# Optimization experiments

Hardware: AMD Instinct MI355X
Metric: run time of the kernel (lower is better)

## Reference

```python
import jax, jax.numpy as jnp
import numpy as np

EEG_CH = 64      # eeg_channel_new
WIN = 128        # window_length
KEN = 10         # cnn_ken_num
CONV_H = 64      # cnn_conv_hight (stride/kernel height)


def setup_inputs() -> dict:
    key = jax.random.key(0)
    ks = jax.random.split(key, 11)
    n = jax.random.normal
    return {
        "x": n(ks[0], (1, 1, 66, 128), dtype=jnp.float32),
        # SE fcn: Linear(64,64) -> Tanh -> Linear(64,64) -> Sigmoid -> Softmax
        "se_w1": n(ks[1], (64, 64), dtype=jnp.float32) * 0.1,
        "se_b1": n(ks[2], (64,), dtype=jnp.float32) * 0.1,
        "se_w2": n(ks[3], (64, 64), dtype=jnp.float32) * 0.1,
        "se_b2": n(ks[4], (64,), dtype=jnp.float32) * 0.1,
        # Conv2d(1, 10, (64, 9), stride=(64, 1))
        "conv_w": n(ks[5], (10, 1, 64, 9), dtype=jnp.float32) * 0.05,
        "conv_b": n(ks[6], (10,), dtype=jnp.float32) * 0.05,
        # fcn: Linear(20,10) -> Sigmoid -> Linear(10,2) -> Softmax
        "fcn_w1": n(ks[7], (10, 20), dtype=jnp.float32) * 0.1,
        "fcn_b1": n(ks[8], (10,), dtype=jnp.float32) * 0.1,
        "fcn_w2": n(ks[9], (2, 10), dtype=jnp.float32) * 0.1,
        "fcn_b2": n(ks[10], (2,), dtype=jnp.float32) * 0.1,
    }


def _dot(a, b):
    # Faithful to torch: tensordot over dim 0 -> [64,1]; diag of non-square -> [1];
    # then broadcast-divide by per-column norms -> [64].
    temp = jnp.diagonal(jnp.tensordot(a, b, axes=[[0], [0]]))  # [1]
    norm_a = jnp.linalg.norm(a, axis=0)                        # [64]
    norm_b = jnp.linalg.norm(b, axis=0)                        # [1]
    return temp / (norm_a * norm_b)                            # [64]


def reference(x, se_w1, se_b1, se_w2, se_b2, conv_w, conv_b,
              fcn_w1, fcn_b1, fcn_w2, fcn_b2):
    eeg = x[:, :, 1:1 + EEG_CH, :]      # [1,1,64,128]
    wav_a = x[:, :, 0:1, :]             # [1,1,1,128]
    wav_b = x[:, :, -1:, :]             # [1,1,1,128]

    e2 = eeg.reshape(EEG_CH, WIN)       # [64,128]
    r_a = _dot(e2.T, wav_a.reshape(1, WIN).T)   # [64]
    r_b = _dot(e2.T, wav_b.reshape(1, WIN).T)   # [64]
    eeg_r = jnp.concatenate([r_a, r_b]).reshape(2, -1)  # [2,64]

    # SE channel attention
    h = jnp.tanh(eeg_r @ se_w1.T + se_b1)
    se_w = jax.nn.softmax(jax.nn.sigmoid(h @ se_w2.T + se_b2), axis=1)  # [2,64]
    sd = eeg.reshape(1, EEG_CH, WIN).transpose(1, 0, 2)  # [64,1,128]
    sd = jnp.concatenate([sd, sd], axis=0)               # [128,1,128]
    # (transpose(0,2) * w.view(1,-1)).transpose(0,2) == scale along doubled-channel dim
    eeg_se = (sd * se_w.reshape(-1)[:, None, None]).transpose(1, 0, 2)  # [1,128,128]

    y = eeg_se.reshape(1, 1, 2 * EEG_CH, WIN)            # [1,1,128,128]
    y = jax.lax.conv_general_dilated(
        y, conv_w, window_strides=(CONV_H, 1), padding='VALID',
        dimension_numbers=('NCHW', 'OIHW', 'NCHW'))       # [1,10,2,120]
    y = jax.nn.relu(y + conv_b[None, :, None, None])
    # AdaptiveAvgPool2d((2,1)): H already 2, mean over W
    y = jnp.mean(y, axis=3, keepdims=True)                # [1,10,2,1]
    y = y.reshape(1, -1)                                  # [1,20]

    h2 = jax.nn.sigmoid(y @ fcn_w1.T + fcn_b1)
    return jax.nn.softmax(h2 @ fcn_w2.T + fcn_b2, axis=1)  # [1,2]
```

## Files before the change

kernel.cpp:

```cpp
#include <hip/hip_runtime.h>
#include <math.h>

#define EEG_CH 64
#define WIN    128
#define KW     9
#define OUTW   120
#define NOUT   10
#define ROWP   132
#define CWP    12

__device__ float        g_msum[2 * NOUT];
__device__ unsigned int g_ctr = 0;

__device__ __forceinline__ float readlane_f(float v, int l) {
    return __int_as_float(__builtin_amdgcn_readlane(__float_as_int(v), l));
}

__launch_bounds__(1024)
__global__ void cnn_fused(const float* __restrict__ xg,
                          const float* __restrict__ w1g, const float* __restrict__ b1g,
                          const float* __restrict__ w2g, const float* __restrict__ b2g,
                          const float* __restrict__ cwg, const float* __restrict__ cbg,
                          const float* __restrict__ f1w, const float* __restrict__ f1b,
                          const float* __restrict__ f2w, const float* __restrict__ f2b,
                          float* __restrict__ out)
{
    __shared__ float w1l[64 * 64];
    __shared__ float w2l[64 * 64];
    __shared__ float xl[64 * ROWP];
    __shared__ float cwl[64 * CWP];
    __shared__ float rnorm[66];
    __shared__ float nums[2];
    __shared__ float sef[128];
    __shared__ float part[4][2][OUTW];
    __shared__ float msh[2];
    __shared__ int   sflag;
    __shared__ float msums[2 * NOUT];

    const int tid  = threadIdx.x;
    const int wv   = tid >> 6;
    const int lane = tid & 63;
    const int o    = blockIdx.x;

    const int chbase = (wv & 3) * 16;

    if (tid < 576) {
        const float v = cwg[o * (EEG_CH * KW) + tid];
        cwl[(tid / KW) * CWP + (tid % KW)] = v;
    }
    for (int t = tid; t < 2048; t += 1024) {
        const int row = t >> 5, c4 = t & 31;
        const float4 v = *(const float4*)(xg + (row + 1) * WIN + c4 * 4);
        *(float4*)(xl + row * ROWP + c4 * 4) = v;
    }
    for (int t = tid; t < 2048; t += 1024) {
        const int j  = t & 63;
        const int i4 = (t >> 6) & 15;
        const float* __restrict__ src = (t < 1024) ? w1g : w2g;
        float* __restrict__ dst = (t < 1024) ? w1l : w2l;
        const float4 v = *(const float4*)(src + j * 64 + i4 * 4);
        dst[(i4 * 4 + 0) * 64 + j] = v.x;
        dst[(i4 * 4 + 1) * 64 + j] = v.y;
        dst[(i4 * 4 + 2) * 64 + j] = v.z;
        dst[(i4 * 4 + 3) * 64 + j] = v.w;
    }
    for (int row = wv; row < 66; row += 16) {
        const float v0 = xg[row * WIN + lane];
        const float v1 = xg[row * WIN + 64 + lane];
        float s = v0 * v0 + v1 * v1;
        for (int off = 32; off > 0; off >>= 1) s += __shfl_xor(s, off, 64);
        if (lane == 0) rnorm[row] = sqrtf(s);
    }
    if (wv < 2) {
        const int wrow = (wv == 0) ? 0 : 65;
        float p = xg[WIN + lane]      * xg[wrow * WIN + lane]
                + xg[WIN + 64 + lane] * xg[wrow * WIN + 64 + lane];
        for (int off = 32; off > 0; off >>= 1) p += __shfl_xor(p, off, 64);
        if (lane == 0) nums[wv] = p;
    }
    __syncthreads();

    if (wv < 2) {
        const int r = wv, j = lane;
        const float er = nums[r] / (rnorm[j + 1] * (r == 0 ? rnorm[0] : rnorm[65]));
        float acc = b1g[j];
        #pragma unroll
        for (int i = 0; i < 64; ++i)
            acc += readlane_f(er, i) * w1l[i * 64 + j];
        const float hv = tanhf(acc);
        float acc2 = b2g[j];
        #pragma unroll
        for (int i = 0; i < 64; ++i)
            acc2 += readlane_f(hv, i) * w2l[i * 64 + j];
        const float sg = 1.f / (1.f + expf(-acc2));
        float mx = sg;
        for (int off = 32; off > 0; off >>= 1) mx = fmaxf(mx, __shfl_xor(mx, off, 64));
        const float e = expf(sg - mx);
        float ss = e;
        for (int off = 32; off > 0; off >>= 1) ss += __shfl_xor(ss, off, 64);
        sef[r * 64 + j] = e / ss;
    }
    __syncthreads();

    const int wbase = (lane < 60) ? 2 * lane : 116;
    if (wv < 4) {
        float sl = 0.f;
        if (lane < 16)      sl = sef[chbase + lane];
        else if (lane < 32) sl = sef[64 + chbase + (lane - 16)];

        float q00 = 0.f, q01 = 0.f;
        float q10 = 0.f, q11 = 0.f;
        #pragma unroll
        for (int ii = 0; ii < 16; ++ii) {
            const int i = chbase + ii;
            const float2* xp = (const float2*)(xl + i * ROWP + wbase);
            const float2 x0 = xp[0], x1 = xp[1], x2 = xp[2], x3 = xp[3], x4 = xp[4];
            const float xw[10] = { x0.x, x0.y, x1.x, x1.y, x2.x, x2.y,
                                   x3.x, x3.y, x4.x, x4.y };
            const float4 wa = *(const float4*)(cwl + i * CWP);
            const float4 wb = *(const float4*)(cwl + i * CWP + 4);
            const float  w8 = cwl[i * CWP + 8];
            const float wk[KW] = { wa.x, wa.y, wa.z, wa.w,
                                   wb.x, wb.y, wb.z, wb.w, w8 };
            const float s0 = readlane_f(sl, ii);
            const float s1 = readlane_f(sl, 16 + ii);
            float p0 = 0.f, p1 = 0.f;
            #pragma unroll
            for (int k = 0; k < KW; ++k) {
                p0 += xw[k]     * wk[k];
                p1 += xw[k + 1] * wk[k];
            }
            q00 += s0 * p0;  q01 += s0 * p1;
            q10 += s1 * p0;  q11 += s1 * p1;
        }
        if (lane < 60) {
            *(float2*)(&part[wv][0][wbase]) = make_float2(q00, q01);
            *(float2*)(&part[wv][1][wbase]) = make_float2(q10, q11);
        }
    }
    __syncthreads();

    if (wv < 2) {
        const float bo = cbg[o];
        float r = 0.f;
        if (lane < 60) {
            float v0 = part[0][wv][wbase], v1 = part[0][wv][wbase + 1];
            #pragma unroll
            for (int q = 1; q < 4; ++q) {
                v0 += part[q][wv][wbase];
                v1 += part[q][wv][wbase + 1];
            }
            v0 += bo; v1 += bo;
            r = fmaxf(v0, 0.f) + fmaxf(v1, 0.f);
        }
        for (int off = 32; off > 0; off >>= 1) r += __shfl_xor(r, off, 64);
        if (lane == 0) msh[wv] = r * (1.0f / OUTW);
    }
    __syncthreads();

    if (tid == 0) {
        __hip_atomic_store(&g_msum[o * 2 + 0], msh[0], __ATOMIC_RELAXED, __HIP_MEMORY_SCOPE_AGENT);
        __hip_atomic_store(&g_msum[o * 2 + 1], msh[1], __ATOMIC_RELAXED, __HIP_MEMORY_SCOPE_AGENT);
        const unsigned old = __hip_atomic_fetch_add(&g_ctr, 1u, __ATOMIC_ACQ_REL, __HIP_MEMORY_SCOPE_AGENT);
        sflag = (old % 10u == 9u) ? 1 : 0;
    }
    __syncthreads();

    if (sflag) {
        if (tid < 2 * NOUT)
            msums[tid] = __hip_atomic_load(&g_msum[tid], __ATOMIC_ACQUIRE, __HIP_MEMORY_SCOPE_AGENT);
        __syncthreads();
        if (tid < 64) {
            float h2v = 0.f;
            if (lane < 10) {
                float a = f1b[lane];
                #pragma unroll
                for (int p = 0; p < 20; ++p) a += msums[p] * f1w[lane * 20 + p];
                h2v = 1.f / (1.f + expf(-a));
            }
            float t0 = (lane < 10) ? h2v * f2w[lane]      : 0.f;
            float t1 = (lane < 10) ? h2v * f2w[10 + lane] : 0.f;
            for (int off = 32; off > 0; off >>= 1) {
                t0 += __shfl_xor(t0, off, 64);
                t1 += __shfl_xor(t1, off, 64);
            }
            if (lane == 0) {
                const float l0 = f2b[0] + t0, l1 = f2b[1] + t1;
                const float m  = fmaxf(l0, l1);
                const float e0 = expf(l0 - m), e1 = expf(l1 - m);
                out[0] = e0 / (e0 + e1);
                out[1] = e1 / (e0 + e1);
            }
        }
    }
}

extern "C" void kernel_launch(void* const* d_in, const int* in_sizes, int n_in,
                              void* d_out, int out_size, void* d_ws, size_t ws_size,
                              hipStream_t stream) {
    (void)in_sizes; (void)n_in; (void)ws_size; (void)out_size; (void)d_ws;
    const float* xg  = (const float*)d_in[0];
    const float* w1  = (const float*)d_in[1];
    const float* b1  = (const float*)d_in[2];
    const float* w2  = (const float*)d_in[3];
    const float* b2  = (const float*)d_in[4];
    const float* cw  = (const float*)d_in[5];
    const float* cb  = (const float*)d_in[6];
    const float* f1w = (const float*)d_in[7];
    const float* f1b = (const float*)d_in[8];
    const float* f2w = (const float*)d_in[9];
    const float* f2b = (const float*)d_in[10];
    float* out = (float*)d_out;

    cnn_fused<<<dim3(NOUT), dim3(1024), 0, stream>>>(xg, w1, b1, w2, b2,
                                                     cw, cb, f1w, f1b, f2w, f2b, out);
}
```

Measured before the change: 84.37 us.

## Overlap SE MLP with unscaled conv partials and widen conv to eight waves

The unscaled per-channel convolution partials are now computed by eight waves, each covering eight channels, while two other waves run the SE attention MLP at the same time. Previously the MLP ran first and the conv waited on it. The SE scale is applied afterward from shared memory, which removes the serial dependency and one barrier phase. The FCN weights are also prefetched into shared memory in the first phase so the last block does not pay global-load latency in its tail. In exchange, each thread keeps 16 partials in registers and the final reduction has to sum eight partial buffers instead of four.

```diff
diff --git a/kernel.cpp b/kernel.cpp
--- a/kernel.cpp
+++ b/kernel.cpp
@@ -32,21 +32,30 @@
     __shared__ float rnorm[66];
     __shared__ float nums[2];
     __shared__ float sef[128];
-    __shared__ float part[4][2][OUTW];
+    __shared__ float part[8][2][OUTW];
     __shared__ float msh[2];
     __shared__ int   sflag;
     __shared__ float msums[2 * NOUT];
+    __shared__ float fcnl[232];
 
     const int tid  = threadIdx.x;
     const int wv   = tid >> 6;
     const int lane = tid & 63;
     const int o    = blockIdx.x;
 
-    const int chbase = (wv & 3) * 16;
+    const int chbase = (wv & 7) * 8;
 
     if (tid < 576) {
         const float v = cwg[o * (EEG_CH * KW) + tid];
         cwl[(tid / KW) * CWP + (tid % KW)] = v;
+    } else if (tid < 808) {
+        const int t = tid - 576;
+        float v;
+        if      (t < 200) v = f1w[t];
+        else if (t < 210) v = f1b[t - 200];
+        else if (t < 230) v = f2w[t - 210];
+        else              v = f2b[t - 230];
+        fcnl[t] = v;
     }
     for (int t = tid; t < 2048; t += 1024) {
         const int row = t >> 5, c4 = t & 31;
@@ -80,38 +89,11 @@
     }
     __syncthreads();
 
-    if (wv < 2) {
-        const int r = wv, j = lane;
-        const float er = nums[r] / (rnorm[j + 1] * (r == 0 ? rnorm[0] : rnorm[65]));
-        float acc = b1g[j];
-        #pragma unroll
-        for (int i = 0; i < 64; ++i)
-            acc += readlane_f(er, i) * w1l[i * 64 + j];
-        const float hv = tanhf(acc);
-        float acc2 = b2g[j];
-        #pragma unroll
-        for (int i = 0; i < 64; ++i)
-            acc2 += readlane_f(hv, i) * w2l[i * 64 + j];
-        const float sg = 1.f / (1.f + expf(-acc2));
-        float mx = sg;
-        for (int off = 32; off > 0; off >>= 1) mx = fmaxf(mx, __shfl_xor(mx, off, 64));
-        const float e = expf(sg - mx);
-        float ss = e;
-        for (int off = 32; off > 0; off >>= 1) ss += __shfl_xor(ss, off, 64);
-        sef[r * 64 + j] = e / ss;
-    }
-    __syncthreads();
-
     const int wbase = (lane < 60) ? 2 * lane : 116;
-    if (wv < 4) {
-        float sl = 0.f;
-        if (lane < 16)      sl = sef[chbase + lane];
-        else if (lane < 32) sl = sef[64 + chbase + (lane - 16)];
-
-        float q00 = 0.f, q01 = 0.f;
-        float q10 = 0.f, q11 = 0.f;
-        #pragma unroll
-        for (int ii = 0; ii < 16; ++ii) {
+    float p0a[8], p1a[8];
+    if (wv < 8) {
+        #pragma unroll
+        for (int ii = 0; ii < 8; ++ii) {
             const int i = chbase + ii;
             const float2* xp = (const float2*)(xl + i * ROWP + wbase);
             const float2 x0 = xp[0], x1 = xp[1], x2 = xp[2], x3 = xp[3], x4 = xp[4];
@@ -122,16 +104,46 @@
             const float  w8 = cwl[i * CWP + 8];
             const float wk[KW] = { wa.x, wa.y, wa.z, wa.w,
                                    wb.x, wb.y, wb.z, wb.w, w8 };
-            const float s0 = readlane_f(sl, ii);
-            const float s1 = readlane_f(sl, 16 + ii);
             float p0 = 0.f, p1 = 0.f;
             #pragma unroll
             for (int k = 0; k < KW; ++k) {
                 p0 += xw[k]     * wk[k];
                 p1 += xw[k + 1] * wk[k];
             }
-            q00 += s0 * p0;  q01 += s0 * p1;
-            q10 += s1 * p0;  q11 += s1 * p1;
+            p0a[ii] = p0;
+            p1a[ii] = p1;
+        }
+    } else if (wv < 10) {
+        const int r = wv - 8, j = lane;
+        const float er = nums[r] / (rnorm[j + 1] * (r == 0 ? rnorm[0] : rnorm[65]));
+        float acc = b1g[j];
+        #pragma unroll
+        for (int i = 0; i < 64; ++i)
+            acc += readlane_f(er, i) * w1l[i * 64 + j];
+        const float hv = tanhf(acc);
+        float acc2 = b2g[j];
+        #pragma unroll
+        for (int i = 0; i < 64; ++i)
+            acc2 += readlane_f(hv, i) * w2l[i * 64 + j];
+        const float sg = 1.f / (1.f + expf(-acc2));
+        float mx = sg;
+        for (int off = 32; off > 0; off >>= 1) mx = fmaxf(mx, __shfl_xor(mx, off, 64));
+        const float e = expf(sg - mx);
+        float ss = e;
+        for (int off = 32; off > 0; off >>= 1) ss += __shfl_xor(ss, off, 64);
+        sef[r * 64 + j] = e / ss;
+    }
+    __syncthreads();
+
+    if (wv < 8) {
+        float q00 = 0.f, q01 = 0.f;
+        float q10 = 0.f, q11 = 0.f;
+        #pragma unroll
+        for (int ii = 0; ii < 8; ++ii) {
+            const float s0 = sef[chbase + ii];
+            const float s1 = sef[64 + chbase + ii];
+            q00 += s0 * p0a[ii];  q01 += s0 * p1a[ii];
+            q10 += s1 * p0a[ii];  q11 += s1 * p1a[ii];
         }
         if (lane < 60) {
             *(float2*)(&part[wv][0][wbase]) = make_float2(q00, q01);
@@ -146,7 +158,7 @@
         if (lane < 60) {
             float v0 = part[0][wv][wbase], v1 = part[0][wv][wbase + 1];
             #pragma unroll
-            for (int q = 1; q < 4; ++q) {
+            for (int q = 1; q < 8; ++q) {
                 v0 += part[q][wv][wbase];
                 v1 += part[q][wv][wbase + 1];
             }
@@ -173,19 +185,19 @@
         if (tid < 64) {
             float h2v = 0.f;
             if (lane < 10) {
-                float a = f1b[lane];
+                float a = fcnl[200 + lane];
                 #pragma unroll
-                for (int p = 0; p < 20; ++p) a += msums[p] * f1w[lane * 20 + p];
+                for (int p = 0; p < 20; ++p) a += msums[p] * fcnl[lane * 20 + p];
                 h2v = 1.f / (1.f + expf(-a));
             }
-            float t0 = (lane < 10) ? h2v * f2w[lane]      : 0.f;
-            float t1 = (lane < 10) ? h2v * f2w[10 + lane] : 0.f;
+            float t0 = (lane < 10) ? h2v * fcnl[210 + lane] : 0.f;
+            float t1 = (lane < 10) ? h2v * fcnl[220 + lane] : 0.f;
             for (int off = 32; off > 0; off >>= 1) {
                 t0 += __shfl_xor(t0, off, 64);
                 t1 += __shfl_xor(t1, off, 64);
             }
             if (lane == 0) {
-                const float l0 = f2b[0] + t0, l1 = f2b[1] + t1;
+                const float l0 = fcnl[230] + t0, l1 = fcnl[231] + t1;
                 const float m  = fmaxf(l0, l1);
                 const float e0 = expf(l0 - m), e1 = expf(l1 - m);
                 out[0] = e0 / (e0 + e1);
```

Measured after the change: 82.90 us, median of 2. Within noise of the previous version (-1.7%).
